# Kernel optimization log

Measured on AMD Instinct MI355X. Metric: run time of the kernel, lower is better.

## Reference

```python
import jax, jax.numpy as jnp
import numpy as np

B, L, D = 8, 1024, 768
H, W, Dd = 16, 16, 4          # token grid, H*W*Dd == L
N, R, K = 16, 48, 4           # d_state, dt_rank, d_conv
EPS = 1e-5


def _physical_pos_embed(batch_params, has_velocity):
    # physical coords [B, L, 3]: (distance, angle, velocity/time)
    h_idx = jnp.arange(H, dtype=jnp.float32)[None, :, None, None]
    w_idx = jnp.arange(W, dtype=jnp.float32)[None, None, :, None]
    d_idx = jnp.arange(Dd, dtype=jnp.float32)[None, None, None, :]
    rres = batch_params[:, 0][:, None, None, None]
    ares = batch_params[:, 1][:, None, None, None]
    vres = batch_params[:, 2][:, None, None, None]
    zero = jnp.zeros((1, H, W, Dd), jnp.float32)
    dist = h_idx * rres + zero
    ang = (w_idx - W / 2) * ares + zero
    vel = jnp.where(has_velocity[:, None, None, None],
                    (d_idx - Dd / 2) * vres, d_idx * vres) + zero
    coords = jnp.stack([dist, ang, vel], axis=-1).reshape(B, L, 3)
    mx = coords.max(axis=1, keepdims=True)
    mn = coords.min(axis=1, keepdims=True)
    rng = mx - mn
    rng = jnp.where(rng > 0, rng, jnp.ones_like(rng))
    coords = (coords - mn) / rng
    # sincos embed: D/3 = 256 dims per coord (even -> pure sin/cos)
    fdim = D // 3
    omega = jnp.arange(fdim // 2, dtype=jnp.float32) / (fdim / 2.0)
    omega = 1.0 / (10000.0 ** omega)                      # [128]
    out = jnp.einsum('blc,f->blcf', coords, omega)        # [B,L,3,128]
    emb = jnp.concatenate([jnp.sin(out), jnp.cos(out)], axis=-1)  # [B,L,3,256]
    return emb.reshape(B, L, D)


def _rmsnorm(x, w):
    return x * jax.lax.rsqrt(jnp.mean(x * x, axis=-1, keepdims=True) + EPS) * w


def _mamba(h, in_proj_w, in_proj_b, conv_w, conv_b, x_proj_w,
           dt_proj_w, dt_proj_b, A_log, D_param, out_proj_w, out_proj_b):
    xz = h @ in_proj_w.T + in_proj_b                      # [B,L,2D]
    x_in, z = xz[..., :D], xz[..., D:]
    # causal depthwise conv1d, kernel K
    xp = jnp.pad(x_in, ((0, 0), (K - 1, 0), (0, 0)))
    x_conv = sum(xp[:, k:k + L, :] * conv_w[:, 0, k] for k in range(K))
    x_conv = jax.nn.silu(x_conv + conv_b)
    x_dbl = x_conv @ x_proj_w.T                           # [B,L,R+2N]
    dt, Bm, Cm = x_dbl[..., :R], x_dbl[..., R:R + N], x_dbl[..., R + N:]
    dt = jax.nn.softplus(dt @ dt_proj_w.T + dt_proj_b)    # [B,L,D]
    A = -jnp.exp(A_log)                                   # [D,N]
    dA = jnp.exp(dt[..., None] * A)                       # [B,L,D,N]
    dBx = dt[..., None] * Bm[:, :, None, :] * x_conv[..., None]

    def step(hst, inp):
        dA_t, dBx_t, C_t = inp
        hst = dA_t * hst + dBx_t                          # [B,D,N]
        y_t = jnp.einsum('bdn,bn->bd', hst, C_t)
        return hst, y_t

    h0 = jnp.zeros((B, D, N), x_in.dtype)
    _, ys = jax.lax.scan(step, h0, (dA.transpose(1, 0, 2, 3),
                                    dBx.transpose(1, 0, 2, 3),
                                    Cm.transpose(1, 0, 2)))
    y = ys.transpose(1, 0, 2) + D_param * x_conv          # [B,L,D]
    y = y * jax.nn.silu(z)
    return y @ out_proj_w.T + out_proj_b


def reference(x, batch_params, has_velocity, norm_w, in_proj_w, in_proj_b,
              conv_w, conv_b, x_proj_w, dt_proj_w, dt_proj_b, A_log,
              D_param, out_proj_w, out_proj_b):
    pos = _physical_pos_embed(batch_params, has_velocity)
    residual = x + pos                                    # ARBlock residual
    hidden = _rmsnorm(residual, norm_w)
    hidden = _mamba(hidden, in_proj_w, in_proj_b, conv_w, conv_b, x_proj_w,
                    dt_proj_w, dt_proj_b, A_log, D_param,
                    out_proj_w, out_proj_b)
    return hidden + residual


def setup_inputs():
    key = jax.random.key(0)
    ks = jax.random.split(key, 12)
    s = 0.02
    return {
        'x': jax.random.normal(ks[0], (B, L, D), jnp.float32),
        'batch_params': jax.random.uniform(ks[1], (B, 4), jnp.float32, 0.01, 1.0),
        'has_velocity': jax.random.randint(ks[2], (B,), 0, 2) > 0,
        'norm_w': jnp.ones((D,), jnp.float32),
        'in_proj_w': jax.random.normal(ks[3], (2 * D, D), jnp.float32) * s,
        'in_proj_b': jnp.zeros((2 * D,), jnp.float32),
        'conv_w': jax.random.normal(ks[4], (D, 1, K), jnp.float32) * 0.3,
        'conv_b': jnp.zeros((D,), jnp.float32),
        'x_proj_w': jax.random.normal(ks[5], (R + 2 * N, D), jnp.float32) * s,
        'dt_proj_w': jax.random.normal(ks[6], (D, R), jnp.float32) * s,
        'dt_proj_b': jax.random.normal(ks[7], (D,), jnp.float32) * 0.1,
        'A_log': jnp.log(jax.random.uniform(ks[8], (D, N), jnp.float32, 1.0, 16.0)),
        'D_param': jnp.ones((D,), jnp.float32),
        'out_proj_w': jax.random.normal(ks[9], (D, D), jnp.float32) * s,
        'out_proj_b': jnp.zeros((D,), jnp.float32),
    }
```

## Files before the change

kernel.cpp:

```cpp
#include <hip/hip_runtime.h>
#include <math.h>

#define BB 8
#define LL 1024
#define DD 768
#define NNs 16
#define RR 48

typedef __attribute__((ext_vector_type(8))) short bf16x8;
typedef __attribute__((ext_vector_type(4))) float f32x4;
typedef __attribute__((ext_vector_type(2))) float f32x2;

__device__ __forceinline__ float silu_f(float v) { return v / (1.0f + __expf(-v)); }

__device__ __forceinline__ short f2bf(float f) {
    union { float f; unsigned u; } v; v.f = f;
    unsigned r = (v.u + 0x7fffu + ((v.u >> 16) & 1u)) >> 16;
    return (short)r;
}

__device__ __forceinline__ float exp2_fast(float x) {
    float r;
    asm("v_exp_f32 %0, %1" : "=v"(r) : "v"(x));
    return r;
}

__device__ __forceinline__ f32x2 pk_fma(f32x2 a, f32x2 b, f32x2 c) {
    f32x2 d;
    asm("v_pk_fma_f32 %0, %1, %2, %3" : "=v"(d) : "v"(a), "v"(b), "v"(c));
    return d;
}
__device__ __forceinline__ f32x2 pk_mul(f32x2 a, f32x2 b) {
    f32x2 d;
    asm("v_pk_mul_f32 %0, %1, %2" : "=v"(d) : "v"(a), "v"(b));
    return d;
}

__device__ __forceinline__ void async16(const void* g, void* l) {
    __builtin_amdgcn_global_load_lds((const __attribute__((address_space(1))) void*)g,
                                     (__attribute__((address_space(3))) void*)l,
                                     16, 0, 0);
}

__global__ __launch_bounds__(256) void k_cvt2(const float* __restrict__ s1,
                                              short* __restrict__ d1, int n1,
                                              const float* __restrict__ s2,
                                              short* __restrict__ d2, int n2) {
    int i = blockIdx.x * 256 + threadIdx.x;
    if (i < n1) {
        float4 v = ((const float4*)s1)[i];
        short4 o = { f2bf(v.x), f2bf(v.y), f2bf(v.z), f2bf(v.w) };
        ((short4*)d1)[i] = o;
    } else {
        int j = i - n1;
        if (j < n2) {
            float4 v = ((const float4*)s2)[j];
            short4 o = { f2bf(v.x), f2bf(v.y), f2bf(v.z), f2bf(v.w) };
            ((short4*)d2)[j] = o;
        }
    }
}

__global__ __launch_bounds__(256) void k_pos_rms(const float* __restrict__ x,
                                                 const float* __restrict__ norm_w,
                                                 float* __restrict__ res,
                                                 short* __restrict__ hidb) {
    int row = blockIdx.x;
    int l = row & (LL - 1);
    int d3 = l & 3;
    int w = (l >> 2) & 15;
    int h = l >> 6;
    float coord[3] = { h * (1.0f / 15.0f), w * (1.0f / 15.0f), d3 * (1.0f / 3.0f) };
    const float LOG1E4 = 9.210340371976184f;
    int t = threadIdx.x;
    float r[3];
    float s = 0.0f;
#pragma unroll
    for (int i = 0; i < 3; i++) {
        int j = t + i * 256;
        int c = j >> 8;
        int fp = j & 255;
        int f = fp & 127;
        float omega = __expf(-(f * (1.0f / 128.0f)) * LOG1E4);
        float arg = coord[c] * omega;
        float pv = (fp < 128) ? __sinf(arg) : __cosf(arg);
        float rv = x[(size_t)row * DD + j] + pv;
        r[i] = rv;
        s += rv * rv;
    }
#pragma unroll
    for (int off = 32; off; off >>= 1) s += __shfl_xor(s, off, 64);
    __shared__ float ls[4];
    if ((t & 63) == 0) ls[t >> 6] = s;
    __syncthreads();
    s = ls[0] + ls[1] + ls[2] + ls[3];
    float rs = rsqrtf(s * (1.0f / DD) + 1e-5f);
#pragma unroll
    for (int i = 0; i < 3; i++) {
        int j = t + i * 256;
        res[(size_t)row * DD + j] = r[i];
        hidb[(size_t)row * DD + j] = f2bf(r[i] * rs * norm_w[j]);
    }
}

template <int EPI, bool AF32>
__global__ __launch_bounds__(256) void gemm_mfma(const void* __restrict__ Ap,
                                                 const short* __restrict__ Bw,
                                                 int Kd,
                                                 const float* __restrict__ bias,
                                                 const float* __restrict__ resid,
                                                 float* __restrict__ C0,
                                                 float* __restrict__ C1) {
    __shared__ short As[4096];
    __shared__ short Bs[4096];
    int m0 = blockIdx.y * 128;
    int n0 = blockIdx.x * 128;
    int tid = threadIdx.x;
    int lane = tid & 63, wave = tid >> 6;
    int q = lane >> 4, r = lane & 15;
    int wm = wave >> 1, wn = wave & 1;

    const size_t Kb = (size_t)Kd * 2;
    const char* gB0 = (const char*)Bw + (size_t)(n0 + wave * 16 + r) * Kb + q * 16;
    const char* gB1 = gB0 + 64 * Kb;
    char* lB0 = (char*)Bs + wave * 1024;
    char* lB1 = lB0 + 4096;
    const char* gA0 = nullptr; const char* gA1 = nullptr;
    char* lA0 = nullptr; char* lA1 = nullptr;
    if (!AF32) {
        gA0 = (const char*)Ap + (size_t)(m0 + wave * 16 + r) * Kb + q * 16;
        gA1 = gA0 + 64 * Kb;
        lA0 = (char*)As + wave * 1024;
        lA1 = lA0 + 4096;
    }

    f32x4 acc[4][4] = {};

    for (int k0 = 0; k0 < Kd; k0 += 32) {
        if (AF32) {
            const float* Af = (const float*)Ap;
#pragma unroll
            for (int p = 0; p < 2; p++) {
                int m = m0 + (p * 4 + wave) * 16 + r;
                const float* src = Af + (size_t)m * Kd + k0 + q * 8;
                float4 v0 = *(const float4*)src;
                float4 v1 = *(const float4*)(src + 4);
                bf16x8 pk;
                pk[0] = f2bf(v0.x); pk[1] = f2bf(v0.y);
                pk[2] = f2bf(v0.z); pk[3] = f2bf(v0.w);
                pk[4] = f2bf(v1.x); pk[5] = f2bf(v1.y);
                pk[6] = f2bf(v1.z); pk[7] = f2bf(v1.w);
                *(bf16x8*)&As[p * 2048 + wave * 512 + lane * 8] = pk;
            }
        } else {
            async16(gA0, lA0); async16(gA1, lA1);
            gA0 += 64; gA1 += 64;
        }
        async16(gB0, lB0); async16(gB1, lB1);
        gB0 += 64; gB1 += 64;
        __syncthreads();
        bf16x8 af[4], bf[4];
#pragma unroll
        for (int a = 0; a < 4; a++)
            af[a] = *(const bf16x8*)&As[((wm * 4 + a) * 64 + q * 16 + r) * 8];
#pragma unroll
        for (int b = 0; b < 4; b++)
            bf[b] = *(const bf16x8*)&Bs[((wn * 4 + b) * 64 + q * 16 + r) * 8];
#pragma unroll
        for (int a = 0; a < 4; a++)
#pragma unroll
            for (int b = 0; b < 4; b++)
                acc[a][b] = __builtin_amdgcn_mfma_f32_16x16x32_bf16(
                    af[a], bf[b], acc[a][b], 0, 0, 0);
        __syncthreads();
    }

#pragma unroll
    for (int a = 0; a < 4; a++) {
        int mrow = m0 + (wm * 4 + a) * 16 + q * 4;
#pragma unroll
        for (int b = 0; b < 4; b++) {
            int ncol = n0 + (wn * 4 + b) * 16 + r;
            float bb = bias[ncol];
            if (EPI == 1) {
                float* dst = (ncol < DD) ? (C0 + (size_t)mrow * DD + ncol)
                                         : (C1 + (size_t)mrow * DD + (ncol - DD));
#pragma unroll
                for (int e = 0; e < 4; e++)
                    dst[(size_t)e * DD] = acc[a][b][e] + bb;
            } else {
#pragma unroll
                for (int e = 0; e < 4; e++) {
                    size_t idx = (size_t)(mrow + e) * DD + ncol;
                    C0[idx] = acc[a][b][e] + bb + resid[idx];
                }
            }
        }
    }
}

__global__ __launch_bounds__(256) void k_xproj(const float* __restrict__ A,
                                               const float* __restrict__ Bw,
                                               float* __restrict__ C0) {
    __shared__ __align__(16) float As[16][33];
    __shared__ __align__(16) float Bsx[16][81];
    int m0 = blockIdx.x * 32;
    int tid = threadIdx.x;
    int tx = tid & 15, ty = tid >> 4;
    float acc[2][5] = {};
    for (int k0 = 0; k0 < DD; k0 += 16) {
        if (tid < 128) {
            int row = tid >> 2, kq = (tid & 3) * 4;
            float4 v = *(const float4*)(A + (size_t)(m0 + row) * DD + k0 + kq);
            As[kq + 0][row] = v.x; As[kq + 1][row] = v.y;
            As[kq + 2][row] = v.z; As[kq + 3][row] = v.w;
        }
        for (int idx = tid; idx < 320; idx += 256) {
            int row = idx >> 2, kq = (idx & 3) * 4;
            float4 v = *(const float4*)(Bw + (size_t)row * DD + k0 + kq);
            Bsx[kq + 0][row] = v.x; Bsx[kq + 1][row] = v.y;
            Bsx[kq + 2][row] = v.z; Bsx[kq + 3][row] = v.w;
        }
        __syncthreads();
#pragma unroll
        for (int kk = 0; kk < 16; kk++) {
            float a0 = As[kk][ty * 2], a1 = As[kk][ty * 2 + 1];
            float b0 = Bsx[kk][tx * 5 + 0];
            float b1 = Bsx[kk][tx * 5 + 1];
            float b2 = Bsx[kk][tx * 5 + 2];
            float b3 = Bsx[kk][tx * 5 + 3];
            float b4 = Bsx[kk][tx * 5 + 4];
            acc[0][0] += a0 * b0; acc[0][1] += a0 * b1; acc[0][2] += a0 * b2;
            acc[0][3] += a0 * b3; acc[0][4] += a0 * b4;
            acc[1][0] += a1 * b0; acc[1][1] += a1 * b1; acc[1][2] += a1 * b2;
            acc[1][3] += a1 * b3; acc[1][4] += a1 * b4;
        }
        __syncthreads();
    }
#pragma unroll
    for (int i = 0; i < 2; i++) {
        int m = m0 + ty * 2 + i;
#pragma unroll
        for (int j = 0; j < 5; j++)
            C0[(size_t)m * 80 + tx * 5 + j] = acc[i][j];
    }
}

template <int MODE>
__global__ __launch_bounds__(256) void gemm_nt(const float* __restrict__ A, int lda,
                                               const float* __restrict__ Bw, int ldb,
                                               int N, int Kd,
                                               const float* __restrict__ bias,
                                               float* __restrict__ C0, int ldc) {
    __shared__ __align__(16) float As[16][68];
    __shared__ __align__(16) float Bs[16][68];
    int m0 = blockIdx.y * 64;
    int n0 = blockIdx.x * 64;
    int t = threadIdx.x;
    int tx = t & 15, ty = t >> 4;
    int ar = t >> 2;
    int ak = (t & 3) * 4;
    float acc[4][4] = {};
    for (int k0 = 0; k0 < Kd; k0 += 16) {
        float4 av = *(const float4*)(A + (size_t)(m0 + ar) * lda + k0 + ak);
        int brow = n0 + ar;
        if (brow >= N) brow = N - 1;
        float4 bv = *(const float4*)(Bw + (size_t)brow * ldb + k0 + ak);
        As[ak + 0][ar] = av.x; As[ak + 1][ar] = av.y;
        As[ak + 2][ar] = av.z; As[ak + 3][ar] = av.w;
        Bs[ak + 0][ar] = bv.x; Bs[ak + 1][ar] = bv.y;
        Bs[ak + 2][ar] = bv.z; Bs[ak + 3][ar] = bv.w;
        __syncthreads();
#pragma unroll
        for (int kk = 0; kk < 16; kk++) {
            float4 a4 = *(const float4*)&As[kk][ty * 4];
            float4 b4 = *(const float4*)&Bs[kk][tx * 4];
            float aa[4] = { a4.x, a4.y, a4.z, a4.w };
            float bb[4] = { b4.x, b4.y, b4.z, b4.w };
#pragma unroll
            for (int i = 0; i < 4; i++)
#pragma unroll
                for (int j = 0; j < 4; j++) acc[i][j] += aa[i] * bb[j];
        }
        __syncthreads();
    }
    {
        float4 bi = *(const float4*)(bias + n0 + tx * 4);
        float bl[4] = { bi.x, bi.y, bi.z, bi.w };
#pragma unroll
        for (int i = 0; i < 4; i++) {
            int m = m0 + ty * 4 + i;
            float v[4];
#pragma unroll
            for (int j = 0; j < 4; j++) {
                float u = acc[i][j] + bl[j];
                v[j] = (u > 20.0f) ? u : log1pf(__expf(u));
            }
            float4 o = { v[0], v[1], v[2], v[3] };
            *(float4*)(C0 + (size_t)m * DD + n0 + tx * 4) = o;
        }
    }
}

__global__ __launch_bounds__(256) void k_conv(const float* __restrict__ xin,
                                              const float* __restrict__ cw,
                                              const float* __restrict__ cb,
                                              float* __restrict__ xc) {
    size_t g4 = (size_t)blockIdx.x * 256 + threadIdx.x;
    int d = (int)((g4 * 4) % DD);
    int bt = (int)(g4 * 4 / DD);
    int tt = bt & (LL - 1);
    const float* p = xin + (size_t)bt * DD + d;
    float4 zr = { 0.f, 0.f, 0.f, 0.f };
    float4 x0 = (tt >= 3) ? *(const float4*)(p - 3 * DD) : zr;
    float4 x1 = (tt >= 2) ? *(const float4*)(p - 2 * DD) : zr;
    float4 x2 = (tt >= 1) ? *(const float4*)(p - 1 * DD) : zr;
    float4 x3 = *(const float4*)p;
    const float4* cw4 = (const float4*)cw;
    float4 w0 = cw4[d + 0], w1 = cw4[d + 1], w2 = cw4[d + 2], w3 = cw4[d + 3];
    float4 cbv = *(const float4*)(cb + d);
    float4 o;
    o.x = silu_f(cbv.x + x0.x * w0.x + x1.x * w0.y + x2.x * w0.z + x3.x * w0.w);
    o.y = silu_f(cbv.y + x0.y * w1.x + x1.y * w1.y + x2.y * w1.z + x3.y * w1.w);
    o.z = silu_f(cbv.z + x0.z * w2.x + x1.z * w2.y + x2.z * w2.z + x3.z * w2.w);
    o.w = silu_f(cbv.w + x0.w * w3.x + x1.w * w3.y + x2.w * w3.z + x3.w * w3.w);
    *(float4*)(xc + g4 * 4) = o;
}

template <bool YB>
__global__ __launch_bounds__(256, 3) void k_scan(const float* __restrict__ dtf,
                                                 const float* __restrict__ xc,
                                                 const float* __restrict__ xdbl,
                                                 const float* __restrict__ A_log,
                                                 const float* __restrict__ Dp,
                                                 float* __restrict__ zy,
                                                 short* __restrict__ yb) {
    __shared__ float Pl[32 * 8 * 16];
    __shared__ float Sl[32 * 8 * 16];
    int bid = blockIdx.x;
    int xcd = bid & 7;
    int v = bid >> 3;
    int dtile = xcd * 12 + (v % 12);
    int b = v / 12;
    int d0 = dtile * 8;
    int tid = threadIdx.x;
    int dl = tid & 7;
    int c = tid >> 3;
    int d = d0 + dl;

    const float LOG2E = 1.4426950408889634f;
    f32x2 Ac2[8];
    {
        const float4* al = (const float4*)(A_log + d * NNs);
#pragma unroll
        for (int i = 0; i < 4; i++) {
            float4 v4 = al[i];
            Ac2[i * 2]     = (f32x2){ -__expf(v4.x) * LOG2E, -__expf(v4.y) * LOG2E };
            Ac2[i * 2 + 1] = (f32x2){ -__expf(v4.z) * LOG2E, -__expf(v4.w) * LOG2E };
        }
    }
    size_t rb = ((size_t)(b * LL + c * 32)) * DD + d;
    const float* dtp = dtf + rb;
    const float* xcp = xc + rb;
    float* zp = zy + rb;
    short* ybp = yb + rb;
    const float* xrow = xdbl + ((size_t)(b * LL + c * 32)) * 80 + RR;

    f32x2 S2[8];
#pragma unroll
    for (int k = 0; k < 8; k++) S2[k] = (f32x2){ 0.0f, 0.0f };
    float dtsum = 0.0f;
    {
        float dt0 = dtp[0], xc0 = xcp[0];
        float dt1 = dtp[DD], xc1 = xcp[DD];
        float4 Bb[4];
#pragma unroll
        for (int qq = 0; qq < 4; qq++) Bb[qq] = *(const float4*)(xrow + qq * 4);
        for (int i = 0; i < 32; i++) {
            int i2 = (i + 2 < 32) ? i + 2 : 31;
            int i1 = (i + 1 < 32) ? i + 1 : 31;
            float dt2 = dtp[(size_t)i2 * DD];
            float xc2 = xcp[(size_t)i2 * DD];
            float4 nB[4];
            const float* nBr = xrow + i1 * 80;
#pragma unroll
            for (int qq = 0; qq < 4; qq++) nB[qq] = *(const float4*)(nBr + qq * 4);

            float dx = dt0 * xc0;
            dtsum += dt0;
            f32x2 dtp2 = (f32x2){ dt0, dt0 };
            f32x2 dx2 = (f32x2){ dx, dx };
#pragma unroll
            for (int k = 0; k < 8; k++) {
                float4 qb = Bb[k >> 1];
                f32x2 bl2 = (k & 1) ? (f32x2){ qb.z, qb.w } : (f32x2){ qb.x, qb.y };
                f32x2 arg = pk_mul(dtp2, Ac2[k]);
                f32x2 e2;
                e2[0] = exp2_fast(arg[0]);
                e2[1] = exp2_fast(arg[1]);
                f32x2 dxb = pk_mul(dx2, bl2);
                S2[k] = pk_fma(e2, S2[k], dxb);
            }
            dt0 = dt1; dt1 = dt2;
            xc0 = xc1; xc1 = xc2;
#pragma unroll
            for (int qq = 0; qq < 4; qq++) Bb[qq] = nB[qq];
        }
    }
    {
        float* pw = &Pl[(c * 8 + dl) * 16];
        float* sw = &Sl[(c * 8 + dl) * 16];
#pragma unroll
        for (int q2 = 0; q2 < 4; q2++) {
            float4 pv = { exp2_fast(Ac2[q2 * 2][0] * dtsum),
                          exp2_fast(Ac2[q2 * 2][1] * dtsum),
                          exp2_fast(Ac2[q2 * 2 + 1][0] * dtsum),
                          exp2_fast(Ac2[q2 * 2 + 1][1] * dtsum) };
            float4 sv = { S2[q2 * 2][0], S2[q2 * 2][1],
                          S2[q2 * 2 + 1][0], S2[q2 * 2 + 1][1] };
            *(float4*)(pw + q2 * 4) = pv;
            *(float4*)(sw + q2 * 4) = sv;
        }
    }
    __syncthreads();
    if (tid < 128) {
        int d2 = tid >> 4, n2 = tid & 15;
        float hh = 0.0f;
#pragma unroll
        for (int cc = 0; cc < 32; cc++) {
            int idx = (cc * 8 + d2) * 16 + n2;
            float Pv = Pl[idx], Sv = Sl[idx];
            Pl[idx] = hh;
            hh = Pv * hh + Sv;
        }
    }
    __syncthreads();
    f32x2 h2[8];
    {
        const float* hr = &Pl[(c * 8 + dl) * 16];
#pragma unroll
        for (int q2 = 0; q2 < 4; q2++) {
            float4 v4 = *(const float4*)(hr + q2 * 4);
            h2[q2 * 2]     = (f32x2){ v4.x, v4.y };
            h2[q2 * 2 + 1] = (f32x2){ v4.z, v4.w };
        }
    }
    float Dv = Dp[d];
    {
        float dt0 = dtp[0], xc0 = xcp[0], zv0 = zp[0];
        float dt1 = dtp[DD], xc1 = xcp[DD], zv1 = zp[DD];
        float4 Bb[4], Cc[4];
#pragma unroll
        for (int qq = 0; qq < 4; qq++) {
            Bb[qq] = *(const float4*)(xrow + qq * 4);
            Cc[qq] = *(const float4*)(xrow + 16 + qq * 4);
        }
        for (int i = 0; i < 32; i++) {
            int i2 = (i + 2 < 32) ? i + 2 : 31;
            int i1 = (i + 1 < 32) ? i + 1 : 31;
            float dt2 = dtp[(size_t)i2 * DD];
            float xc2 = xcp[(size_t)i2 * DD];
            float zv2 = zp[(size_t)i2 * DD];
            float4 nB[4], nC[4];
            const float* nBr = xrow + i1 * 80;
#pragma unroll
            for (int qq = 0; qq < 4; qq++) {
                nB[qq] = *(const float4*)(nBr + qq * 4);
                nC[qq] = *(const float4*)(nBr + 16 + qq * 4);
            }
            float dx = dt0 * xc0;
            f32x2 dtp2 = (f32x2){ dt0, dt0 };
            f32x2 dx2 = (f32x2){ dx, dx };
            f32x2 y2 = (f32x2){ Dv * xc0, 0.0f };
#pragma unroll
            for (int k = 0; k < 8; k++) {
                float4 qb = Bb[k >> 1];
                float4 qc = Cc[k >> 1];
                f32x2 bl2 = (k & 1) ? (f32x2){ qb.z, qb.w } : (f32x2){ qb.x, qb.y };
                f32x2 cl2 = (k & 1) ? (f32x2){ qc.z, qc.w } : (f32x2){ qc.x, qc.y };
                f32x2 arg = pk_mul(dtp2, Ac2[k]);
                f32x2 e2;
                e2[0] = exp2_fast(arg[0]);
                e2[1] = exp2_fast(arg[1]);
                f32x2 dxb = pk_mul(dx2, bl2);
                h2[k] = pk_fma(e2, h2[k], dxb);
                y2 = pk_fma(h2[k], cl2, y2);
            }
            float y = y2[0] + y2[1];
            float gated = y * silu_f(zv0);
            if (YB) ybp[(size_t)i * DD] = f2bf(gated);
            else    zp[(size_t)i * DD] = gated;
            dt0 = dt1; dt1 = dt2;
            xc0 = xc1; xc1 = xc2;
            zv0 = zv1; zv1 = zv2;
#pragma unroll
            for (int qq = 0; qq < 4; qq++) { Bb[qq] = nB[qq]; Cc[qq] = nC[qq]; }
        }
    }
}

extern "C" void kernel_launch(void* const* d_in, const int* in_sizes, int n_in,
                              void* d_out, int out_size, void* d_ws, size_t ws_size,
                              hipStream_t stream) {
    const float* x      = (const float*)d_in[0];
    const float* norm_w = (const float*)d_in[3];
    const float* in_w   = (const float*)d_in[4];
    const float* in_b   = (const float*)d_in[5];
    const float* conv_w = (const float*)d_in[6];
    const float* conv_b = (const float*)d_in[7];
    const float* xp_w   = (const float*)d_in[8];
    const float* dt_w   = (const float*)d_in[9];
    const float* dt_b   = (const float*)d_in[10];
    const float* A_log  = (const float*)d_in[11];
    const float* Dp     = (const float*)d_in[12];
    const float* out_w  = (const float*)d_in[13];
    const float* out_b  = (const float*)d_in[14];
    float* out = (float*)d_out;

    const size_t S = (size_t)BB * LL * DD;
    float* res   = (float*)d_ws;
    float* slotA = res + S;
    float* slotB = slotA + S;
    float* zf    = slotB + S;
    float* xdbl  = zf + S;
    short* inw_b  = (short*)(xdbl + (size_t)BB * LL * 80);
    short* outw_b = inw_b + 1536 * DD;
    short* ybf    = outw_b + DD * DD;

    short* hidb = (short*)slotA;
    float* xc   = slotA;
    float* xin  = slotB;
    float* dtf  = slotB;

    const int M = BB * LL;

    size_t need = (size_t)((char*)(ybf + S) - (char*)d_ws);
    bool useYB = ws_size >= need;

    {
        int n1 = 1536 * DD / 4, n2 = DD * DD / 4;
        k_cvt2<<<(n1 + n2 + 255) / 256, 256, 0, stream>>>(in_w, inw_b, n1,
                                                          out_w, outw_b, n2);
    }

    k_pos_rms<<<M, 256, 0, stream>>>(x, norm_w, res, hidb);

    gemm_mfma<1, false><<<dim3(1536 / 128, M / 128), 256, 0, stream>>>(
        hidb, inw_b, DD, in_b, nullptr, xin, zf);

    k_conv<<<(int)(S / 1024), 256, 0, stream>>>(xin, conv_w, conv_b, xc);

    k_xproj<<<M / 32, 256, 0, stream>>>(xc, xp_w, xdbl);

    gemm_nt<2><<<dim3(DD / 64, M / 64), 256, 0, stream>>>(
        xdbl, 80, dt_w, RR, DD, RR, dt_b, dtf, DD);

    if (useYB) {
        k_scan<true><<<768, 256, 0, stream>>>(dtf, xc, xdbl, A_log, Dp, zf, ybf);
        gemm_mfma<3, false><<<dim3(DD / 128, M / 128), 256, 0, stream>>>(
            ybf, outw_b, DD, out_b, res, out, nullptr);
    } else {
        k_scan<false><<<768, 256, 0, stream>>>(dtf, xc, xdbl, A_log, Dp, zf, ybf);
        gemm_mfma<3, true><<<dim3(DD / 128, M / 128), 256, 0, stream>>>(
            zf, outw_b, DD, out_b, res, out, nullptr);
    }
}
```

Measured before the change: 366.9 us.

## Split x_proj GEMM over K with atomic accumulation and larger row tiles

The x_proj GEMM (8192x80x768) now splits the K dimension into 8 chunks of 96 across a 2D grid, uses 64-row tiles with 4x5 outputs per thread, and accumulates partial sums into the output with atomicAdd. The output buffer is zeroed inside the conv kernel so no extra launch is needed. This is meant to raise the block count and per-thread arithmetic intensity of a skinny GEMM that previously ran only 256 blocks over the full K. In exchange it adds float atomic traffic and makes the summation order nondeterministic.

After: 411.1 us. 12.1% more time.

```diff
diff --git a/kernel.cpp b/kernel.cpp
--- a/kernel.cpp
+++ b/kernel.cpp
@@ -202,47 +202,50 @@
 __global__ __launch_bounds__(256) void k_xproj(const float* __restrict__ A,
                                                const float* __restrict__ Bw,
                                                float* __restrict__ C0) {
-    __shared__ __align__(16) float As[16][33];
-    __shared__ __align__(16) float Bsx[16][81];
-    int m0 = blockIdx.x * 32;
-    int tid = threadIdx.x;
-    int tx = tid & 15, ty = tid >> 4;
-    float acc[2][5] = {};
-    for (int k0 = 0; k0 < DD; k0 += 16) {
-        if (tid < 128) {
-            int row = tid >> 2, kq = (tid & 3) * 4;
-            float4 v = *(const float4*)(A + (size_t)(m0 + row) * DD + k0 + kq);
-            As[kq + 0][row] = v.x; As[kq + 1][row] = v.y;
-            As[kq + 2][row] = v.z; As[kq + 3][row] = v.w;
-        }
-        for (int idx = tid; idx < 320; idx += 256) {
+    __shared__ __align__(16) float As[16][68];
+    __shared__ __align__(16) float Bs[16][84];
+    int kbase = blockIdx.x * 96;
+    int m0 = blockIdx.y * 64;
+    int t = threadIdx.x;
+    int tx = t & 15, ty = t >> 4;
+    int ar = t >> 2;
+    int ak = (t & 3) * 4;
+    float acc[4][5] = {};
+    for (int k0 = kbase; k0 < kbase + 96; k0 += 16) {
+        float4 av = *(const float4*)(A + (size_t)(m0 + ar) * DD + k0 + ak);
+        As[ak + 0][ar] = av.x; As[ak + 1][ar] = av.y;
+        As[ak + 2][ar] = av.z; As[ak + 3][ar] = av.w;
+        for (int idx = t; idx < 320; idx += 256) {
             int row = idx >> 2, kq = (idx & 3) * 4;
-            float4 v = *(const float4*)(Bw + (size_t)row * DD + k0 + kq);
-            Bsx[kq + 0][row] = v.x; Bsx[kq + 1][row] = v.y;
-            Bsx[kq + 2][row] = v.z; Bsx[kq + 3][row] = v.w;
+            float4 bv = *(const float4*)(Bw + (size_t)row * DD + k0 + kq);
+            Bs[kq + 0][row] = bv.x; Bs[kq + 1][row] = bv.y;
+            Bs[kq + 2][row] = bv.z; Bs[kq + 3][row] = bv.w;
         }
         __syncthreads();
 #pragma unroll
         for (int kk = 0; kk < 16; kk++) {
-            float a0 = As[kk][ty * 2], a1 = As[kk][ty * 2 + 1];
-            float b0 = Bsx[kk][tx * 5 + 0];
-            float b1 = Bsx[kk][tx * 5 + 1];
-            float b2 = Bsx[kk][tx * 5 + 2];
-            float b3 = Bsx[kk][tx * 5 + 3];
-            float b4 = Bsx[kk][tx * 5 + 4];
-            acc[0][0] += a0 * b0; acc[0][1] += a0 * b1; acc[0][2] += a0 * b2;
-            acc[0][3] += a0 * b3; acc[0][4] += a0 * b4;
-            acc[1][0] += a1 * b0; acc[1][1] += a1 * b1; acc[1][2] += a1 * b2;
-            acc[1][3] += a1 * b3; acc[1][4] += a1 * b4;
+            float4 a4 = *(const float4*)&As[kk][ty * 4];
+            float aa[4] = { a4.x, a4.y, a4.z, a4.w };
+            float b0 = Bs[kk][tx * 5 + 0];
+            float b1 = Bs[kk][tx * 5 + 1];
+            float b2 = Bs[kk][tx * 5 + 2];
+            float b3 = Bs[kk][tx * 5 + 3];
+            float b4 = Bs[kk][tx * 5 + 4];
+#pragma unroll
+            for (int i = 0; i < 4; i++) {
+                acc[i][0] += aa[i] * b0; acc[i][1] += aa[i] * b1;
+                acc[i][2] += aa[i] * b2; acc[i][3] += aa[i] * b3;
+                acc[i][4] += aa[i] * b4;
+            }
         }
         __syncthreads();
     }
 #pragma unroll
-    for (int i = 0; i < 2; i++) {
-        int m = m0 + ty * 2 + i;
+    for (int i = 0; i < 4; i++) {
+        int m = m0 + ty * 4 + i;
 #pragma unroll
         for (int j = 0; j < 5; j++)
-            C0[(size_t)m * 80 + tx * 5 + j] = acc[i][j];
+            atomicAdd(C0 + (size_t)m * 80 + tx * 5 + j, acc[i][j]);
     }
 }
 
@@ -305,8 +308,13 @@
 __global__ __launch_bounds__(256) void k_conv(const float* __restrict__ xin,
                                               const float* __restrict__ cw,
                                               const float* __restrict__ cb,
-                                              float* __restrict__ xc) {
+                                              float* __restrict__ xc,
+                                              float* __restrict__ xdbl) {
     size_t g4 = (size_t)blockIdx.x * 256 + threadIdx.x;
+    if (g4 < (size_t)BB * LL * 80 / 4) {
+        float4 zr4 = { 0.f, 0.f, 0.f, 0.f };
+        ((float4*)xdbl)[g4] = zr4;
+    }
     int d = (int)((g4 * 4) % DD);
     int bt = (int)(g4 * 4 / DD);
     int tt = bt & (LL - 1);
@@ -548,9 +556,9 @@
     gemm_mfma<1, false><<<dim3(1536 / 128, M / 128), 256, 0, stream>>>(
         hidb, inw_b, DD, in_b, nullptr, xin, zf);
 
-    k_conv<<<(int)(S / 1024), 256, 0, stream>>>(xin, conv_w, conv_b, xc);
-
-    k_xproj<<<M / 32, 256, 0, stream>>>(xc, xp_w, xdbl);
+    k_conv<<<(int)(S / 1024), 256, 0, stream>>>(xin, conv_w, conv_b, xc, xdbl);
+
+    k_xproj<<<dim3(8, M / 64), 256, 0, stream>>>(xc, xp_w, xdbl);
 
     gemm_nt<2><<<dim3(DD / 64, M / 64), 256, 0, stream>>>(
         xdbl, 80, dt_w, RR, DD, RR, dt_b, dtf, DD);
```
